# Performance work log

Measured on AMD Instinct MI355X. Metric: run time of the kernel, lower is better.

## Reference

```python
import jax, jax.numpy as jnp
import numpy as np

N, D = 16384, 2048

def setup_inputs() -> dict:
    key = jax.random.key(0)
    k1, k2, k3 = jax.random.split(key, 3)
    x1 = jax.random.normal(k1, (N, D), dtype=jnp.float32)
    x2 = jax.random.normal(k2, (N, D), dtype=jnp.float32)
    w = jax.random.normal(k3, (D,), dtype=jnp.float32)
    return {"x1": x1, "x2": x2, "w": w}

def reference(x1, x2, w):
    # per-row attention scores: s_k[i] = dot(x_k[i], w)
    s1 = x1 @ w  # [N]
    s2 = x2 @ w  # [N]
    # alpha_1 = exp(s1)/(exp(s1)+exp(s2)) == sigmoid(s1 - s2) (numerically stable)
    alpha1 = jax.nn.sigmoid(s1 - s2)  # [N]
    alpha2 = 1.0 - alpha1
    fused = alpha1[:, None] * x1 + alpha2[:, None] * x2  # [N, D]
    alpha = jnp.stack([alpha1, alpha2], axis=1)  # [N, 2], detached in original
    return fused, alpha
```

## Files before the change

### kernel.cpp

```cpp
#include <hip/hip_runtime.h>


#define NROWS 16384
#define DCOLS 2048

typedef float f32x4 __attribute__((ext_vector_type(4)));

__device__ __forceinline__ void stage16(const void* g, void* l)
{
    __builtin_amdgcn_global_load_lds(
        (const __attribute__((address_space(1))) void*)g,
        (__attribute__((address_space(3))) void*)l, 16, 0, 0);
}

__global__ __launch_bounds__(256) void attn_fuse_kernel(
    const float* __restrict__ x1,
    const float* __restrict__ x2,
    const float* __restrict__ w,
    float* __restrict__ fused,
    float* __restrict__ alpha)
{
    __shared__ float x1L[DCOLS];
    __shared__ float x2L[DCOLS];
    __shared__ float wsum[4];

    const int t = threadIdx.x;
    const int wave = t >> 6;
    const int lane = t & 63;
    const size_t row = blockIdx.x;

    {
        const char* g1 = (const char*)(x1 + row * DCOLS) + wave * 2048 + lane * 16;
        const char* g2 = (const char*)(x2 + row * DCOLS) + wave * 2048 + lane * 16;
        char* l1 = (char*)x1L + wave * 2048;
        char* l2 = (char*)x2L + wave * 2048;
        stage16(g1,        l1);
        stage16(g1 + 1024, l1 + 1024);
        stage16(g2,        l2);
        stage16(g2 + 1024, l2 + 1024);
    }

    const f32x4* __restrict__ wv = (const f32x4*)w;
    const f32x4 w0 = wv[t];
    const f32x4 w1 = wv[t + 256];

    __syncthreads();

    const f32x4 a0 = ((const f32x4*)x1L)[t];
    const f32x4 a1 = ((const f32x4*)x1L)[t + 256];
    const f32x4 b0 = ((const f32x4*)x2L)[t];
    const f32x4 b1 = ((const f32x4*)x2L)[t + 256];

    float p = 0.0f;
    p = fmaf(a0.x - b0.x, w0.x, p);
    p = fmaf(a0.y - b0.y, w0.y, p);
    p = fmaf(a0.z - b0.z, w0.z, p);
    p = fmaf(a0.w - b0.w, w0.w, p);
    p = fmaf(a1.x - b1.x, w1.x, p);
    p = fmaf(a1.y - b1.y, w1.y, p);
    p = fmaf(a1.z - b1.z, w1.z, p);
    p = fmaf(a1.w - b1.w, w1.w, p);

    #pragma unroll
    for (int off = 32; off > 0; off >>= 1)
        p += __shfl_down(p, off, 64);

    if (lane == 0) wsum[wave] = p;
    __syncthreads();
    const float d = wsum[0] + wsum[1] + wsum[2] + wsum[3];

    const float g = 1.0f / (1.0f + expf(-d));

    f32x4 f0, f1;
    f0.x = fmaf(g, a0.x - b0.x, b0.x);
    f0.y = fmaf(g, a0.y - b0.y, b0.y);
    f0.z = fmaf(g, a0.z - b0.z, b0.z);
    f0.w = fmaf(g, a0.w - b0.w, b0.w);
    f1.x = fmaf(g, a1.x - b1.x, b1.x);
    f1.y = fmaf(g, a1.y - b1.y, b1.y);
    f1.z = fmaf(g, a1.z - b1.z, b1.z);
    f1.w = fmaf(g, a1.w - b1.w, b1.w);

    f32x4* __restrict__ outv = (f32x4*)(fused + row * DCOLS);
    outv[t] = f0;
    outv[t + 256] = f1;

    if (t == 0) {
        alpha[row * 2]     = g;
        alpha[row * 2 + 1] = 1.0f - g;
    }
}

extern "C" void kernel_launch(void* const* d_in, const int* in_sizes, int n_in,
                              void* d_out, int out_size, void* d_ws, size_t ws_size,
                              hipStream_t stream)
{
    const float* x1 = (const float*)d_in[0];
    const float* x2 = (const float*)d_in[1];
    const float* w  = (const float*)d_in[2];

    float* fused = (float*)d_out;
    float* alpha = fused + (size_t)NROWS * DCOLS;

    attn_fuse_kernel<<<NROWS, 256, 0, stream>>>(x1, x2, w, fused, alpha);
}
```

Baseline: 305.1 us.

## Split fused attention kernel into separate dot and blend kernels

Replaces the single row-per-block kernel (LDS staging via global_load_lds) with two kernels. The first computes per-row dot products and the sigmoid gate with direct vector loads and writes only alpha. The second streams x1/x2 with a grid-stride loop and writes the blended output with nontemporal stores. This decouples the reduction from the streaming blend to improve memory-level parallelism, at the cost of reading both inputs twice from memory or cache.

```diff
diff --git a/kernel.cpp b/kernel.cpp
--- a/kernel.cpp
+++ b/kernel.cpp
@@ -3,53 +3,31 @@
 
 #define NROWS 16384
 #define DCOLS 2048
+#define NF4 ((size_t)NROWS * (DCOLS / 4))
 
 typedef float f32x4 __attribute__((ext_vector_type(4)));
 
-__device__ __forceinline__ void stage16(const void* g, void* l)
-{
-    __builtin_amdgcn_global_load_lds(
-        (const __attribute__((address_space(1))) void*)g,
-        (__attribute__((address_space(3))) void*)l, 16, 0, 0);
-}
-
-__global__ __launch_bounds__(256) void attn_fuse_kernel(
+__global__ __launch_bounds__(256) void dot_kernel(
     const float* __restrict__ x1,
     const float* __restrict__ x2,
     const float* __restrict__ w,
-    float* __restrict__ fused,
     float* __restrict__ alpha)
 {
-    __shared__ float x1L[DCOLS];
-    __shared__ float x2L[DCOLS];
-    __shared__ float wsum[4];
-
     const int t = threadIdx.x;
     const int wave = t >> 6;
     const int lane = t & 63;
     const size_t row = blockIdx.x;
 
-    {
-        const char* g1 = (const char*)(x1 + row * DCOLS) + wave * 2048 + lane * 16;
-        const char* g2 = (const char*)(x2 + row * DCOLS) + wave * 2048 + lane * 16;
-        char* l1 = (char*)x1L + wave * 2048;
-        char* l2 = (char*)x2L + wave * 2048;
-        stage16(g1,        l1);
-        stage16(g1 + 1024, l1 + 1024);
-        stage16(g2,        l2);
-        stage16(g2 + 1024, l2 + 1024);
-    }
+    const f32x4* __restrict__ x1v = (const f32x4*)(x1 + row * DCOLS);
+    const f32x4* __restrict__ x2v = (const f32x4*)(x2 + row * DCOLS);
+    const f32x4* __restrict__ wv  = (const f32x4*)w;
 
-    const f32x4* __restrict__ wv = (const f32x4*)w;
+    const f32x4 a0 = x1v[t];
+    const f32x4 a1 = x1v[t + 256];
+    const f32x4 b0 = x2v[t];
+    const f32x4 b1 = x2v[t + 256];
     const f32x4 w0 = wv[t];
     const f32x4 w1 = wv[t + 256];
-
-    __syncthreads();
-
-    const f32x4 a0 = ((const f32x4*)x1L)[t];
-    const f32x4 a1 = ((const f32x4*)x1L)[t + 256];
-    const f32x4 b0 = ((const f32x4*)x2L)[t];
-    const f32x4 b1 = ((const f32x4*)x2L)[t + 256];
 
     float p = 0.0f;
     p = fmaf(a0.x - b0.x, w0.x, p);
@@ -65,29 +43,42 @@
     for (int off = 32; off > 0; off >>= 1)
         p += __shfl_down(p, off, 64);
 
+    __shared__ float wsum[4];
     if (lane == 0) wsum[wave] = p;
     __syncthreads();
-    const float d = wsum[0] + wsum[1] + wsum[2] + wsum[3];
-
-    const float g = 1.0f / (1.0f + expf(-d));
-
-    f32x4 f0, f1;
-    f0.x = fmaf(g, a0.x - b0.x, b0.x);
-    f0.y = fmaf(g, a0.y - b0.y, b0.y);
-    f0.z = fmaf(g, a0.z - b0.z, b0.z);
-    f0.w = fmaf(g, a0.w - b0.w, b0.w);
-    f1.x = fmaf(g, a1.x - b1.x, b1.x);
-    f1.y = fmaf(g, a1.y - b1.y, b1.y);
-    f1.z = fmaf(g, a1.z - b1.z, b1.z);
-    f1.w = fmaf(g, a1.w - b1.w, b1.w);
-
-    f32x4* __restrict__ outv = (f32x4*)(fused + row * DCOLS);
-    outv[t] = f0;
-    outv[t + 256] = f1;
 
     if (t == 0) {
+        const float d = wsum[0] + wsum[1] + wsum[2] + wsum[3];
+        const float g = 1.0f / (1.0f + expf(-d));
         alpha[row * 2]     = g;
         alpha[row * 2 + 1] = 1.0f - g;
+    }
+}
+
+__global__ __launch_bounds__(256) void fuse_kernel(
+    const float* __restrict__ x1,
+    const float* __restrict__ x2,
+    const float* __restrict__ alpha,
+    float* __restrict__ fused)
+{
+    const f32x4* __restrict__ av = (const f32x4*)x1;
+    const f32x4* __restrict__ bv = (const f32x4*)x2;
+    f32x4* __restrict__ ov = (f32x4*)fused;
+
+    const size_t stride = (size_t)gridDim.x * 256;
+    size_t i = (size_t)blockIdx.x * 256 + threadIdx.x;
+
+    #pragma unroll 4
+    for (; i < NF4; i += stride) {
+        const float g = alpha[(i >> 9) << 1];
+        const f32x4 a = av[i];
+        const f32x4 b = bv[i];
+        f32x4 f;
+        f.x = fmaf(g, a.x - b.x, b.x);
+        f.y = fmaf(g, a.y - b.y, b.y);
+        f.z = fmaf(g, a.z - b.z, b.z);
+        f.w = fmaf(g, a.w - b.w, b.w);
+        __builtin_nontemporal_store(f, ov + i);
     }
 }
 
@@ -102,5 +93,6 @@
     float* fused = (float*)d_out;
     float* alpha = fused + (size_t)NROWS * DCOLS;
 
-    attn_fuse_kernel<<<NROWS, 256, 0, stream>>>(x1, x2, w, fused, alpha);
+    dot_kernel<<<NROWS, 256, 0, stream>>>(x1, x2, w, alpha);
+    fuse_kernel<<<2048, 256, 0, stream>>>(x1, x2, alpha, fused);
 }
```

After: 354.3 us. +16.1%, slower.
